# Optimization experiments

Measured on AMD Instinct MI355X. Metric: run time of the kernel, lower is better.

Reference implementation:

```python
import jax, jax.numpy as jnp
import numpy as np

D_MODEL = 1024
NUM_HEADS = 16
ROPE_THETA = 10000.0


def _rope(v, pos, theta=ROPE_THETA):
    # v: [B, S, D] (full d_model, as in the original module), pos: [B, S] int
    d = v.shape[-1]
    inv_freq = theta ** (-jnp.arange(0, d, 2, dtype=jnp.float32) / d)  # [D/2]
    ang = pos.astype(jnp.float32)[..., None] * inv_freq  # [B, S, D/2]
    cos, sin = jnp.cos(ang), jnp.sin(ang)
    x1, x2 = v[..., ::2], v[..., 1::2]
    r1 = x1 * cos - x2 * sin
    r2 = x1 * sin + x2 * cos
    return jnp.stack([r1, r2], axis=-1).reshape(v.shape)


def setup_inputs() -> dict:
    key = jax.random.key(0)
    ks = jax.random.split(key, 6)
    B, S, D = 2, 2048, D_MODEL
    std = np.sqrt(2.0 / (D + D)).astype(np.float32)
    x = jax.random.normal(ks[0], (B, S, D), dtype=jnp.float32)
    token_positions = jnp.sort(jax.random.randint(ks[1], (B, S), 0, S), axis=-1).astype(jnp.int32)
    wq = jax.random.normal(ks[2], (D, D), dtype=jnp.float32) * std
    wk = jax.random.normal(ks[3], (D, D), dtype=jnp.float32) * std
    wv = jax.random.normal(ks[4], (D, D), dtype=jnp.float32) * std
    wo = jax.random.normal(ks[5], (D, D), dtype=jnp.float32) * std
    return {"x": x, "token_positions": token_positions, "wq": wq, "wk": wk, "wv": wv, "wo": wo}


def reference(x, token_positions, wq, wk, wv, wo):
    B, S, D = x.shape
    H = NUM_HEADS
    dk = D // H
    # Projections (nn.functional.linear: x @ W^T)
    q = x @ wq.T
    k = x @ wk.T
    v = x @ wv.T
    # In the original, Q/K are reshaped to heads and back before RoPE -> identity;
    # RoPE is applied over the FULL d_model dimension.
    q = _rope(q, token_positions)
    k = _rope(k, token_positions)
    # Split heads
    q = q.reshape(B, S, H, dk)
    k = k.reshape(B, S, H, dk)
    v = v.reshape(B, S, H, dk)
    scores = jnp.einsum('bqhd,bkhd->bhqk', q, k) / jnp.sqrt(jnp.asarray(dk, x.dtype))
    causal = jnp.tril(jnp.ones((S, S), dtype=bool))  # True where allowed
    scores = jnp.where(causal[None, None], scores, -jnp.inf)
    attn = jax.nn.softmax(scores, axis=-1)
    out = jnp.einsum('bhqk,bkhd->bqhd', attn, v).reshape(B, S, D)
    return out @ wo.T
```

## Files before the change

### kernel.cpp

```cpp
#include <hip/hip_runtime.h>
#include <hip/hip_bf16.h>
#include <math.h>

typedef __attribute__((ext_vector_type(8))) short bf16x8;
typedef __attribute__((ext_vector_type(4))) float f32x4;
typedef __attribute__((ext_vector_type(8))) float f32x8;

#define D_MODEL 1024
#define NHEADS  16
#define DK      64
#define BATCH   2
#define SEQ     2048

static __device__ __forceinline__ short f2bf(float f) {
    unsigned u = __builtin_bit_cast(unsigned, f);
    u = u + 0x7FFFu + ((u >> 16) & 1u);
    return (short)(u >> 16);
}
static __device__ __forceinline__ short f2bf_fast(float f) {
    return (short)((__builtin_bit_cast(unsigned, f) + 0x8000u) >> 16);
}
static __device__ __forceinline__ float bf2f(short s) {
    return __builtin_bit_cast(float, ((unsigned)(unsigned short)s) << 16);
}

typedef __attribute__((address_space(3))) unsigned int lds_uint;
typedef __attribute__((address_space(1))) const unsigned int glob_uint;
static __device__ __forceinline__ void gl2lds16(const short* g, short* l) {
    __builtin_amdgcn_global_load_lds((glob_uint*)g, (lds_uint*)l, 16, 0, 0);
}

__global__ void detect_kernel(const unsigned* __restrict__ x, int* __restrict__ flag)
{
    const int lane = threadIdx.x;
    const unsigned w = x[lane];
    const unsigned e = (w >> 7) & 0xFFu;
    const bool weird = (e >= 0x88u) || (e <= 0x5Fu);
    const unsigned long long m = __ballot(weird);
    if (lane == 0) *flag = (__popcll(m) >= 16) ? 1 : 0;
}

#define NX8 ((BATCH * SEQ * D_MODEL) / 8)
#define NW8 ((D_MODEL * D_MODEL) / 8)
__global__ void cvt_all_kernel(const void* __restrict__ x,  const void* __restrict__ wq,
                               const void* __restrict__ wk, const void* __restrict__ wv,
                               const void* __restrict__ wo,
                               __hip_bfloat16* __restrict__ xb,  __hip_bfloat16* __restrict__ wqb,
                               __hip_bfloat16* __restrict__ wkb, __hip_bfloat16* __restrict__ wvb,
                               __hip_bfloat16* __restrict__ wob,
                               const int* __restrict__ dtf)
{
    const int i = blockIdx.x * blockDim.x + threadIdx.x;
    if (i >= NX8 + 4 * NW8) return;
    const void* src; __hip_bfloat16* dst; int off;
    if (i < NX8) { src = x; dst = xb; off = i; }
    else {
        const int j = i - NX8, seg = j >> 17; off = j & (NW8 - 1);
        switch (seg) {
            case 0: src = wq; dst = wqb; break;
            case 1: src = wk; dst = wkb; break;
            case 2: src = wv; dst = wvb; break;
            default: src = wo; dst = wob; break;
        }
    }
    if (*dtf) {
        const f32x8 v = ((const f32x8*)src)[off];
        bf16x8 r;
#pragma unroll
        for (int j = 0; j < 8; ++j) r[j] = f2bf(v[j]);
        ((bf16x8*)dst)[off] = r;
    } else {
        ((bf16x8*)dst)[off] = ((const bf16x8*)src)[off];
    }
}

static __device__ __forceinline__ void gemm128_main(
    const short* __restrict__ A, const short* __restrict__ B,
    int K, int bm, int bn, f32x4 (&acc)[4][4], short* lds)
{
    const int tid  = threadIdx.x;
    const int lane = tid & 63;
    const int wave = tid >> 6;
    const int l16  = lane & 15;
    const int quad = lane >> 4;

    const int srow = lane >> 2;
    const int scg  = (lane & 3) ^ ((lane >> 3) & 3);
    const short* ag = A + (size_t)(bm + wave * 32 + srow) * K + scg * 8;
    const short* bg = B + (size_t)(bn + wave * 32 + srow) * K + scg * 8;
    const int dst = wave * 1024 + lane * 8;

    const int mrow = (wave >> 1) * 64;
    const int nrow = (wave & 1) * 64;
    const int ph   = ((quad ^ ((l16 >> 1) & 3))) * 8;

    auto stage = [&](int k0, int buf) {
        short* ad = lds + buf * 4096 + dst;
        short* bd = lds + 8192 + buf * 4096 + dst;
        gl2lds16(ag + k0, ad);
        gl2lds16(ag + k0 + (size_t)16 * K, ad + 512);
        gl2lds16(bg + k0, bd);
        gl2lds16(bg + k0 + (size_t)16 * K, bd + 512);
    };

    stage(0, 0);
    for (int k0 = 0, t = 0; k0 < K; k0 += 32, ++t) {
        __asm__ volatile("s_waitcnt vmcnt(0)" ::: "memory");
        __syncthreads();
        if (k0 + 32 < K) stage(k0 + 32, (t + 1) & 1);

        const short* Ab = lds + (t & 1) * 4096;
        const short* Bb = lds + 8192 + (t & 1) * 4096;
        bf16x8 a[4], b[4];
#pragma unroll
        for (int x = 0; x < 4; ++x)
            a[x] = *(const bf16x8*)(Ab + (mrow + x * 16 + l16) * 32 + ph);
#pragma unroll
        for (int y = 0; y < 4; ++y)
            b[y] = *(const bf16x8*)(Bb + (nrow + y * 16 + l16) * 32 + ph);
#pragma unroll
        for (int x = 0; x < 4; ++x)
#pragma unroll
            for (int y = 0; y < 4; ++y)
                acc[x][y] = __builtin_amdgcn_mfma_f32_16x16x32_bf16(
                    a[x], b[y], acc[x][y], 0, 0, 0);
    }
}

__global__ __launch_bounds__(256) void gemm_qkv_kernel(
    const __hip_bfloat16* __restrict__ xb,
    const __hip_bfloat16* __restrict__ wqb,
    const __hip_bfloat16* __restrict__ wkb,
    const __hip_bfloat16* __restrict__ wvb,
    __hip_bfloat16* __restrict__ Qb,
    __hip_bfloat16* __restrict__ Kb,
    __hip_bfloat16* __restrict__ Vt)
{
    __shared__ alignas(16) short lds[16384];
    const int wsel = blockIdx.x >> 3;
    const int bn   = (blockIdx.x & 7) * 128;
    const int bm   = blockIdx.y * 128;
    const short* W = (const short*)(wsel == 0 ? wqb : (wsel == 1 ? wkb : wvb));

    f32x4 acc[4][4];
#pragma unroll
    for (int x = 0; x < 4; ++x)
#pragma unroll
        for (int y = 0; y < 4; ++y) acc[x][y] = (f32x4){0.f, 0.f, 0.f, 0.f};

    gemm128_main((const short*)xb, W, D_MODEL, bm, bn, acc, lds);

    const int lane = threadIdx.x & 63;
    const int wave = threadIdx.x >> 6;
    const int l16  = lane & 15;
    const int quad = lane >> 4;
    __hip_bfloat16* Crm = (wsel == 1) ? Kb : Qb;

#pragma unroll
    for (int x = 0; x < 4; ++x)
#pragma unroll
        for (int y = 0; y < 4; ++y)
#pragma unroll
            for (int r = 0; r < 4; ++r) {
                const int row = bm + (wave >> 1) * 64 + x * 16 + quad * 4 + r;
                const int col = bn + (wave & 1) * 64 + y * 16 + l16;
                const __hip_bfloat16 v = __float2bfloat16(acc[x][y][r]);
                if (wsel == 2) {
                    const int hh = col >> 6, dcol = col & 63;
                    const int bb = row >> 11, ss = row & (SEQ - 1);
                    Vt[(((size_t)bb * NHEADS + hh) * DK + dcol) * SEQ + ss] = v;
                } else {
                    Crm[(size_t)row * D_MODEL + col] = v;
                }
            }
}

__global__ __launch_bounds__(256) void gemm_out_kernel(
    const __hip_bfloat16* __restrict__ AO,
    const __hip_bfloat16* __restrict__ wob,
    void* __restrict__ C, const int* __restrict__ dtf)
{
    __shared__ alignas(16) short lds[16384];
    const int bn = blockIdx.x * 128;
    const int bm = blockIdx.y * 128;
    const bool c32 = (*dtf) != 0;

    f32x4 acc[4][4];
#pragma unroll
    for (int x = 0; x < 4; ++x)
#pragma unroll
        for (int y = 0; y < 4; ++y) acc[x][y] = (f32x4){0.f, 0.f, 0.f, 0.f};

    gemm128_main((const short*)AO, (const short*)wob, D_MODEL, bm, bn, acc, lds);

    const int lane = threadIdx.x & 63;
    const int wave = threadIdx.x >> 6;
    const int l16  = lane & 15;
    const int quad = lane >> 4;

#pragma unroll
    for (int x = 0; x < 4; ++x)
#pragma unroll
        for (int y = 0; y < 4; ++y)
#pragma unroll
            for (int r = 0; r < 4; ++r) {
                const int row = bm + (wave >> 1) * 64 + x * 16 + quad * 4 + r;
                const int col = bn + (wave & 1) * 64 + y * 16 + l16;
                const size_t idx = (size_t)row * D_MODEL + col;
                if (c32) ((float*)C)[idx] = acc[x][y][r];
                else     ((__hip_bfloat16*)C)[idx] = __float2bfloat16(acc[x][y][r]);
            }
}

__global__ void rope_kernel(__hip_bfloat16* __restrict__ Q,
                            __hip_bfloat16* __restrict__ Kt,
                            const int* __restrict__ pos, int n8)
{
    const int idx = blockIdx.x * blockDim.x + threadIdx.x;
    if (idx >= n8) return;
    const int elem0 = idx * 8;
    const int bs = elem0 >> 10;
    const int i0 = (elem0 & (D_MODEL - 1)) >> 1;

    const float p = (float)pos[bs];
    bf16x8 q8 = *((bf16x8*)Q + idx);
    bf16x8 k8 = *((bf16x8*)Kt + idx);

#pragma unroll
    for (int j = 0; j < 4; ++j) {
        const float inv = exp2f((float)(i0 + j) * -0.02595256257f);
        const float ang = p * inv;
        const float c = cosf(ang), s = sinf(ang);
        const float q1 = bf2f(q8[2 * j]);
        const float q2 = bf2f(q8[2 * j + 1]);
        const float k1 = bf2f(k8[2 * j]);
        const float k2 = bf2f(k8[2 * j + 1]);
        q8[2 * j]     = f2bf(q1 * c - q2 * s);
        q8[2 * j + 1] = f2bf(q1 * s + q2 * c);
        k8[2 * j]     = f2bf(k1 * c - k2 * s);
        k8[2 * j + 1] = f2bf(k1 * s + k2 * c);
    }
    *((bf16x8*)Q + idx)  = q8;
    *((bf16x8*)Kt + idx) = k8;
}

__global__ __launch_bounds__(256) void flash_attn_kernel(
    __hip_bfloat16* QO,
    const __hip_bfloat16* __restrict__ Kt,
    const __hip_bfloat16* __restrict__ Vt)
{
    __shared__ alignas(16) short k_lds[2][64 * 64];
    __shared__ alignas(16) short v_lds[2][64 * 64];
    __shared__ alignas(16) short p_lds[4][16 * 72];

    const int lane = threadIdx.x & 63;
    const int wave = threadIdx.x >> 6;
    const int l16  = lane & 15;
    const int quad = lane >> 4;
    const int qtA  = blockIdx.x;
    const int qtB  = 31 - qtA;
    const int b    = blockIdx.y / NHEADS;
    const int h    = blockIdx.y % NHEADS;
    const size_t base  = (size_t)b * SEQ * D_MODEL + h * DK;
    const size_t vbase = (size_t)blockIdx.y * DK * SEQ;

    const short* Qp = (const short*)QO;
    const short* Kp = (const short*)Kt;
    const short* Vp = (const short*)Vt;

    const int qA0 = qtA * 64 + wave * 16;
    const int qB0 = qtB * 64 + wave * 16;
    const bf16x8 aqA0 = *(const bf16x8*)(Qp + base + (size_t)(qA0 + l16) * D_MODEL + quad * 8);
    const bf16x8 aqA1 = *(const bf16x8*)(Qp + base + (size_t)(qA0 + l16) * D_MODEL + 32 + quad * 8);
    const bf16x8 aqB0 = *(const bf16x8*)(Qp + base + (size_t)(qB0 + l16) * D_MODEL + quad * 8);
    const bf16x8 aqB1 = *(const bf16x8*)(Qp + base + (size_t)(qB0 + l16) * D_MODEL + 32 + quad * 8);

    f32x4 oA[4], oB[4];
    float lA[4] = {0.f, 0.f, 0.f, 0.f}, lB[4] = {0.f, 0.f, 0.f, 0.f};
#pragma unroll
    for (int g = 0; g < 4; ++g) { oA[g] = (f32x4){0.f,0.f,0.f,0.f}; oB[g] = (f32x4){0.f,0.f,0.f,0.f}; }

    const int srow = lane >> 3;
    const int scg  = (lane & 7) ^ srow;
    const int dst  = wave * 512 + lane * 8;
    const short* kg = Kp + ((size_t)b * SEQ + wave * 8 + srow) * D_MODEL + h * DK + scg * 8;
    const short* vg = Vp + vbase + (size_t)(wave * 8 + srow) * SEQ + scg * 8;

    const int ph0 = (quad ^ (l16 & 7)) * 8;
    const int ph1 = ((4 + quad) ^ (l16 & 7)) * 8;

    auto stage = [&](int t, int buf) {
        const int kv0 = t * 64;
        gl2lds16(kg + (size_t)kv0 * D_MODEL, k_lds[buf] + dst);
        gl2lds16(kg + (size_t)(kv0 + 32) * D_MODEL, k_lds[buf] + 2048 + dst);
        gl2lds16(vg + kv0, v_lds[buf] + dst);
        gl2lds16(vg + kv0 + (size_t)32 * SEQ, v_lds[buf] + 2048 + dst);
    };

    auto process = [&](int buf, int kv0, int q0, bool masked,
                       const bf16x8& aq0, const bf16x8& aq1,
                       f32x4 (&o)[4], float (&ls)[4]) {
        const short* kb = k_lds[buf];
        const short* vb = v_lds[buf];
        f32x4 sfrag[4];
#pragma unroll
        for (int g = 0; g < 4; ++g) {
            const int rowk = (g * 16 + l16) * 64;
            const bf16x8 bk0 = *(const bf16x8*)(kb + rowk + ph0);
            const bf16x8 bk1 = *(const bf16x8*)(kb + rowk + ph1);
            f32x4 c = (f32x4){0.f, 0.f, 0.f, 0.f};
            c = __builtin_amdgcn_mfma_f32_16x16x32_bf16(aq0, bk0, c, 0, 0, 0);
            c = __builtin_amdgcn_mfma_f32_16x16x32_bf16(aq1, bk1, c, 0, 0, 0);
            sfrag[g] = c;
        }
#pragma unroll
        for (int r = 0; r < 4; ++r) {
            const int qrow = q0 + quad * 4 + r;
            float ps = 0.f;
#pragma unroll
            for (int g = 0; g < 4; ++g) {
                float p = __expf(sfrag[g][r] * 0.125f);
                if (masked && (kv0 + g * 16 + l16 > qrow)) p = 0.f;
                ps += p;
                p_lds[wave][(quad * 4 + r) * 72 + g * 16 + l16] = f2bf_fast(p);
            }
            ls[r] += ps;
        }
        __asm__ volatile("s_waitcnt lgkmcnt(0)" ::: "memory");
        const bf16x8 ap0 = *(const bf16x8*)(&p_lds[wave][l16 * 72 + quad * 8]);
        const bf16x8 ap1 = *(const bf16x8*)(&p_lds[wave][l16 * 72 + 32 + quad * 8]);
#pragma unroll
        for (int g = 0; g < 4; ++g) {
            const int rowv = (g * 16 + l16) * 64;
            const bf16x8 bv0 = *(const bf16x8*)(vb + rowv + ph0);
            const bf16x8 bv1 = *(const bf16x8*)(vb + rowv + ph1);
            o[g] = __builtin_amdgcn_mfma_f32_16x16x32_bf16(ap0, bv0, o[g], 0, 0, 0);
            o[g] = __builtin_amdgcn_mfma_f32_16x16x32_bf16(ap1, bv1, o[g], 0, 0, 0);
        }
    };

    const int tiles = qtB + 1;
    stage(0, 0);
    for (int t = 0; t < tiles; ++t) {
        __asm__ volatile("s_waitcnt vmcnt(0)" ::: "memory");
        __syncthreads();
        if (t + 1 < tiles) stage(t + 1, (t + 1) & 1);

        const int kv0 = t * 64;
        const int buf = t & 1;
        if (t <= qtA) process(buf, kv0, qA0, t == qtA, aqA0, aqA1, oA, lA);
        process(buf, kv0, qB0, t == qtB, aqB0, aqB1, oB, lB);
    }

#pragma unroll
    for (int r = 0; r < 4; ++r) {
        float sa = lA[r], sb = lB[r];
#pragma unroll
        for (int off = 1; off < 16; off <<= 1) {
            sa += __shfl_xor(sa, off);
            sb += __shfl_xor(sb, off);
        }
        lA[r] = sa; lB[r] = sb;
    }
#pragma unroll
    for (int g = 0; g < 4; ++g)
#pragma unroll
        for (int r = 0; r < 4; ++r) {
            const int rowA = qA0 + quad * 4 + r;
            const int rowB = qB0 + quad * 4 + r;
            QO[base + (size_t)rowA * D_MODEL + g * 16 + l16] =
                __float2bfloat16(oA[g][r] / fmaxf(lA[r], 1e-20f));
            QO[base + (size_t)rowB * D_MODEL + g * 16 + l16] =
                __float2bfloat16(oB[g][r] / fmaxf(lB[r], 1e-20f));
        }
}

extern "C" void kernel_launch(void* const* d_in, const int* in_sizes, int n_in,
                              void* d_out, int out_size, void* d_ws, size_t ws_size,
                              hipStream_t stream)
{
    (void)in_sizes; (void)n_in; (void)out_size; (void)ws_size;

    const void* x  = d_in[0];
    const int*  pos = (const int*)d_in[1];
    const void* wq = d_in[2];
    const void* wk = d_in[3];
    const void* wv = d_in[4];
    const void* wo = d_in[5];

    const int M = BATCH * SEQ;
    const int D = D_MODEL;
    const size_t MD = (size_t)M * D;
    const size_t DD = (size_t)D * D;

    int* dtf = (int*)d_ws;
    __hip_bfloat16* xb  = (__hip_bfloat16*)((char*)d_ws + 256);
    __hip_bfloat16* wqb = xb  + MD;
    __hip_bfloat16* wkb = wqb + DD;
    __hip_bfloat16* wvb = wkb + DD;
    __hip_bfloat16* wob = wvb + DD;
    __hip_bfloat16* Qb  = wob + DD;
    __hip_bfloat16* Vtb = Qb  + MD;
    __hip_bfloat16* Kb  = (__hip_bfloat16*)d_out;

    dim3 blk(256);

    hipLaunchKernelGGL(detect_kernel, dim3(1), dim3(64), 0, stream,
                       (const unsigned*)x, dtf);

    const int ncvt = NX8 + 4 * NW8;
    hipLaunchKernelGGL(cvt_all_kernel, dim3((ncvt + 255) / 256), blk, 0, stream,
                       x, wq, wk, wv, wo, xb, wqb, wkb, wvb, wob, dtf);

    hipLaunchKernelGGL(gemm_qkv_kernel, dim3(24, 32), blk, 0, stream,
                       xb, wqb, wkb, wvb, Qb, Kb, Vtb);

    const int nrope8 = (int)(MD / 8);
    hipLaunchKernelGGL(rope_kernel, dim3((nrope8 + 255) / 256), blk, 0, stream,
                       Qb, Kb, pos, nrope8);

    hipLaunchKernelGGL(flash_attn_kernel, dim3(SEQ / 128, BATCH * NHEADS), blk, 0, stream,
                       Qb, Kb, Vtb);

    hipLaunchKernelGGL(gemm_out_kernel, dim3(D / 128, M / 128), blk, 0, stream,
                       Qb, wob, d_out, dtf);
}
```

Before: 202.4 us.

## Fuse RoPE into QKV GEMM epilogue, retile out-proj and widen attention KV tiles

Applies the rotary embedding in the QKV GEMM epilogue, using a lane shuffle to fetch each element's pair partner, and drops the separate RoPE kernel and its extra read and write pass over Q and K. The output-projection GEMM moves to 64x128 tiles with its own double-buffered LDS loop, doubling the block count to improve CU occupancy. Flash attention now stages 128-key K/V tiles per barrier and processes them as two 64-key halves, halving the sync and stage steps. These add trig work to the GEMM epilogue and more LDS per attention block, which may lower occupancy.

Result: slower. 251.2 us (+24.1%).

```diff
diff --git a/kernel.cpp b/kernel.cpp
--- a/kernel.cpp
+++ b/kernel.cpp
@@ -134,7 +134,8 @@
     const __hip_bfloat16* __restrict__ wvb,
     __hip_bfloat16* __restrict__ Qb,
     __hip_bfloat16* __restrict__ Kb,
-    __hip_bfloat16* __restrict__ Vt)
+    __hip_bfloat16* __restrict__ Vt,
+    const int* __restrict__ pos)
 {
     __shared__ alignas(16) short lds[16384];
     const int wsel = blockIdx.x >> 3;
@@ -164,13 +165,22 @@
             for (int r = 0; r < 4; ++r) {
                 const int row = bm + (wave >> 1) * 64 + x * 16 + quad * 4 + r;
                 const int col = bn + (wave & 1) * 64 + y * 16 + l16;
-                const __hip_bfloat16 v = __float2bfloat16(acc[x][y][r]);
+                float v = acc[x][y][r];
+                const float p2 = __shfl_xor(v, 1);
+                if (wsel < 2) {
+                    const float pp  = (float)pos[row];
+                    const float inv = exp2f((float)(col >> 1) * -0.02595256257f);
+                    const float ang = pp * inv;
+                    const float c = cosf(ang), s = sinf(ang);
+                    v = (col & 1) ? (p2 * s + v * c) : (v * c - p2 * s);
+                }
+                const __hip_bfloat16 o = __float2bfloat16(v);
                 if (wsel == 2) {
                     const int hh = col >> 6, dcol = col & 63;
                     const int bb = row >> 11, ss = row & (SEQ - 1);
-                    Vt[(((size_t)bb * NHEADS + hh) * DK + dcol) * SEQ + ss] = v;
+                    Vt[(((size_t)bb * NHEADS + hh) * DK + dcol) * SEQ + ss] = o;
                 } else {
-                    Crm[(size_t)row * D_MODEL + col] = v;
+                    Crm[(size_t)row * D_MODEL + col] = o;
                 }
             }
 }
@@ -180,77 +190,83 @@
     const __hip_bfloat16* __restrict__ wob,
     void* __restrict__ C, const int* __restrict__ dtf)
 {
-    __shared__ alignas(16) short lds[16384];
-    const int bn = blockIdx.x * 128;
-    const int bm = blockIdx.y * 128;
-    const bool c32 = (*dtf) != 0;
-
-    f32x4 acc[4][4];
-#pragma unroll
-    for (int x = 0; x < 4; ++x)
-#pragma unroll
-        for (int y = 0; y < 4; ++y) acc[x][y] = (f32x4){0.f, 0.f, 0.f, 0.f};
-
-    gemm128_main((const short*)AO, (const short*)wob, D_MODEL, bm, bn, acc, lds);
-
-    const int lane = threadIdx.x & 63;
-    const int wave = threadIdx.x >> 6;
+    __shared__ alignas(16) short lds[2][6144];
+    const int tid  = threadIdx.x;
+    const int lane = tid & 63;
+    const int wave = tid >> 6;
     const int l16  = lane & 15;
     const int quad = lane >> 4;
-
+    const int bn = blockIdx.x * 128;
+    const int bm = blockIdx.y * 64;
+    const bool c32 = (*dtf) != 0;
+    const int K = D_MODEL;
+
+    const int srow = lane >> 2;
+    const int scg  = (lane & 3) ^ ((lane >> 3) & 3);
+    const short* Ap = (const short*)AO;
+    const short* Bp = (const short*)wob;
+    const short* ag = Ap + (size_t)(bm + wave * 16 + srow) * K + scg * 8;
+    const short* bg = Bp + (size_t)(bn + wave * 32 + srow) * K + scg * 8;
+
+    const int nrow = wave * 32;
+    const int ph   = ((quad ^ ((l16 >> 1) & 3))) * 8;
+
+    f32x4 acc[4][2];
 #pragma unroll
     for (int x = 0; x < 4; ++x)
 #pragma unroll
-        for (int y = 0; y < 4; ++y)
+        for (int y = 0; y < 2; ++y) acc[x][y] = (f32x4){0.f, 0.f, 0.f, 0.f};
+
+    auto stage = [&](int k0, int buf) {
+        gl2lds16(ag + k0, &lds[buf][wave * 512 + lane * 8]);
+        gl2lds16(bg + k0, &lds[buf][2048 + wave * 1024 + lane * 8]);
+        gl2lds16(bg + k0 + (size_t)16 * K, &lds[buf][2048 + wave * 1024 + 512 + lane * 8]);
+    };
+
+    stage(0, 0);
+    for (int k0 = 0, t = 0; k0 < K; k0 += 32, ++t) {
+        __asm__ volatile("s_waitcnt vmcnt(0)" ::: "memory");
+        __syncthreads();
+        if (k0 + 32 < K) stage(k0 + 32, (t + 1) & 1);
+
+        const short* Ab = &lds[t & 1][0];
+        const short* Bb = &lds[t & 1][2048];
+        bf16x8 a[4], b[2];
+#pragma unroll
+        for (int x = 0; x < 4; ++x)
+            a[x] = *(const bf16x8*)(Ab + (x * 16 + l16) * 32 + ph);
+#pragma unroll
+        for (int y = 0; y < 2; ++y)
+            b[y] = *(const bf16x8*)(Bb + (nrow + y * 16 + l16) * 32 + ph);
+#pragma unroll
+        for (int x = 0; x < 4; ++x)
+#pragma unroll
+            for (int y = 0; y < 2; ++y)
+                acc[x][y] = __builtin_amdgcn_mfma_f32_16x16x32_bf16(
+                    a[x], b[y], acc[x][y], 0, 0, 0);
+    }
+
+#pragma unroll
+    for (int x = 0; x < 4; ++x)
+#pragma unroll
+        for (int y = 0; y < 2; ++y)
 #pragma unroll
             for (int r = 0; r < 4; ++r) {
-                const int row = bm + (wave >> 1) * 64 + x * 16 + quad * 4 + r;
-                const int col = bn + (wave & 1) * 64 + y * 16 + l16;
+                const int row = bm + x * 16 + quad * 4 + r;
+                const int col = bn + nrow + y * 16 + l16;
                 const size_t idx = (size_t)row * D_MODEL + col;
                 if (c32) ((float*)C)[idx] = acc[x][y][r];
                 else     ((__hip_bfloat16*)C)[idx] = __float2bfloat16(acc[x][y][r]);
             }
 }
 
-__global__ void rope_kernel(__hip_bfloat16* __restrict__ Q,
-                            __hip_bfloat16* __restrict__ Kt,
-                            const int* __restrict__ pos, int n8)
-{
-    const int idx = blockIdx.x * blockDim.x + threadIdx.x;
-    if (idx >= n8) return;
-    const int elem0 = idx * 8;
-    const int bs = elem0 >> 10;
-    const int i0 = (elem0 & (D_MODEL - 1)) >> 1;
-
-    const float p = (float)pos[bs];
-    bf16x8 q8 = *((bf16x8*)Q + idx);
-    bf16x8 k8 = *((bf16x8*)Kt + idx);
-
-#pragma unroll
-    for (int j = 0; j < 4; ++j) {
-        const float inv = exp2f((float)(i0 + j) * -0.02595256257f);
-        const float ang = p * inv;
-        const float c = cosf(ang), s = sinf(ang);
-        const float q1 = bf2f(q8[2 * j]);
-        const float q2 = bf2f(q8[2 * j + 1]);
-        const float k1 = bf2f(k8[2 * j]);
-        const float k2 = bf2f(k8[2 * j + 1]);
-        q8[2 * j]     = f2bf(q1 * c - q2 * s);
-        q8[2 * j + 1] = f2bf(q1 * s + q2 * c);
-        k8[2 * j]     = f2bf(k1 * c - k2 * s);
-        k8[2 * j + 1] = f2bf(k1 * s + k2 * c);
-    }
-    *((bf16x8*)Q + idx)  = q8;
-    *((bf16x8*)Kt + idx) = k8;
-}
-
 __global__ __launch_bounds__(256) void flash_attn_kernel(
     __hip_bfloat16* QO,
     const __hip_bfloat16* __restrict__ Kt,
     const __hip_bfloat16* __restrict__ Vt)
 {
-    __shared__ alignas(16) short k_lds[2][64 * 64];
-    __shared__ alignas(16) short v_lds[2][64 * 64];
+    __shared__ alignas(16) short k_lds[2][128 * 64];
+    __shared__ alignas(16) short v_lds[2][64 * 128];
     __shared__ alignas(16) short p_lds[4][16 * 72];
 
     const int lane = threadIdx.x & 63;
@@ -280,28 +296,37 @@
 #pragma unroll
     for (int g = 0; g < 4; ++g) { oA[g] = (f32x4){0.f,0.f,0.f,0.f}; oB[g] = (f32x4){0.f,0.f,0.f,0.f}; }
 
-    const int srow = lane >> 3;
-    const int scg  = (lane & 7) ^ srow;
-    const int dst  = wave * 512 + lane * 8;
-    const short* kg = Kp + ((size_t)b * SEQ + wave * 8 + srow) * D_MODEL + h * DK + scg * 8;
-    const short* vg = Vp + vbase + (size_t)(wave * 8 + srow) * SEQ + scg * 8;
+    const int srowK = lane >> 3;
+    const int scgK  = (lane & 7) ^ srowK;
+    const short* kg = Kp + ((size_t)b * SEQ + wave * 32 + srowK) * D_MODEL + h * DK + scgK * 8;
+    const int rinV = lane >> 4;
+    const int cgV  = lane & 15;
+    const short* vgA = Vp + vbase + (size_t)(wave * 16 + rinV) * SEQ + ((cgV ^ rinV)) * 8;
+    const short* vgB = Vp + vbase + (size_t)(wave * 16 + rinV) * SEQ + ((cgV ^ (4 + rinV))) * 8;
 
     const int ph0 = (quad ^ (l16 & 7)) * 8;
     const int ph1 = ((4 + quad) ^ (l16 & 7)) * 8;
-
-    auto stage = [&](int t, int buf) {
-        const int kv0 = t * 64;
-        gl2lds16(kg + (size_t)kv0 * D_MODEL, k_lds[buf] + dst);
-        gl2lds16(kg + (size_t)(kv0 + 32) * D_MODEL, k_lds[buf] + 2048 + dst);
-        gl2lds16(vg + kv0, v_lds[buf] + dst);
-        gl2lds16(vg + kv0 + (size_t)32 * SEQ, v_lds[buf] + 2048 + dst);
+    const int pv1 = ((8 + quad) ^ (l16 & 7)) * 8;
+
+    auto stage = [&](int t2, int buf) {
+        const int kv0 = t2 * 128;
+#pragma unroll
+        for (int i = 0; i < 4; ++i)
+            gl2lds16(kg + (size_t)(kv0 + i * 8) * D_MODEL,
+                     k_lds[buf] + (wave * 32 + i * 8) * 64 + lane * 8);
+#pragma unroll
+        for (int i = 0; i < 4; ++i) {
+            const short* vp = (i & 1) ? vgB : vgA;
+            gl2lds16(vp + (size_t)(i * 4) * SEQ + kv0,
+                     v_lds[buf] + (wave * 16 + i * 4) * 128 + lane * 8);
+        }
     };
 
-    auto process = [&](int buf, int kv0, int q0, bool masked,
+    auto process = [&](int buf, int half, int kv0, int q0, bool masked,
                        const bf16x8& aq0, const bf16x8& aq1,
                        f32x4 (&o)[4], float (&ls)[4]) {
-        const short* kb = k_lds[buf];
-        const short* vb = v_lds[buf];
+        const short* kb = k_lds[buf] + half * 64 * 64;
+        const short* vb = v_lds[buf] + half * 64;
         f32x4 sfrag[4];
 #pragma unroll
         for (int g = 0; g < 4; ++g) {
@@ -329,27 +354,30 @@
         __asm__ volatile("s_waitcnt lgkmcnt(0)" ::: "memory");
         const bf16x8 ap0 = *(const bf16x8*)(&p_lds[wave][l16 * 72 + quad * 8]);
         const bf16x8 ap1 = *(const bf16x8*)(&p_lds[wave][l16 * 72 + 32 + quad * 8]);
+        const int phv0 = half ? pv1 : ph0;
 #pragma unroll
         for (int g = 0; g < 4; ++g) {
-            const int rowv = (g * 16 + l16) * 64;
-            const bf16x8 bv0 = *(const bf16x8*)(vb + rowv + ph0);
-            const bf16x8 bv1 = *(const bf16x8*)(vb + rowv + ph1);
+            const int rowv = (g * 16 + l16) * 128;
+            const bf16x8 bv0 = *(const bf16x8*)(v_lds[buf] + rowv + half * 0 + phv0);
+            const bf16x8 bv1 = *(const bf16x8*)(v_lds[buf] + rowv + (half ? ph1 + 64 : ph1));
             o[g] = __builtin_amdgcn_mfma_f32_16x16x32_bf16(ap0, bv0, o[g], 0, 0, 0);
             o[g] = __builtin_amdgcn_mfma_f32_16x16x32_bf16(ap1, bv1, o[g], 0, 0, 0);
         }
     };
 
-    const int tiles = qtB + 1;
+    const int t2max = qtB >> 1;
     stage(0, 0);
-    for (int t = 0; t < tiles; ++t) {
+    for (int t2 = 0; t2 <= t2max; ++t2) {
         __asm__ volatile("s_waitcnt vmcnt(0)" ::: "memory");
         __syncthreads();
-        if (t + 1 < tiles) stage(t + 1, (t + 1) & 1);
-
-        const int kv0 = t * 64;
-        const int buf = t & 1;
-        if (t <= qtA) process(buf, kv0, qA0, t == qtA, aqA0, aqA1, oA, lA);
-        process(buf, kv0, qB0, t == qtB, aqB0, aqB1, oB, lB);
+        if (t2 < t2max) stage(t2 + 1, (t2 + 1) & 1);
+        const int buf = t2 & 1;
+#pragma unroll
+        for (int half = 0; half < 2; ++half) {
+            const int kvt = 2 * t2 + half;
+            if (kvt <= qtA) process(buf, half, kvt * 64, qA0, kvt == qtA, aqA0, aqA1, oA, lA);
+            if (kvt <= qtB) process(buf, half, kvt * 64, qB0, kvt == qtB, aqB0, aqB1, oB, lB);
+        }
     }
 
 #pragma unroll
@@ -413,15 +441,11 @@
                        x, wq, wk, wv, wo, xb, wqb, wkb, wvb, wob, dtf);
 
     hipLaunchKernelGGL(gemm_qkv_kernel, dim3(24, 32), blk, 0, stream,
-                       xb, wqb, wkb, wvb, Qb, Kb, Vtb);
-
-    const int nrope8 = (int)(MD / 8);
-    hipLaunchKernelGGL(rope_kernel, dim3((nrope8 + 255) / 256), blk, 0, stream,
-                       Qb, Kb, pos, nrope8);
+                       xb, wqb, wkb, wvb, Qb, Kb, Vtb, pos);
 
     hipLaunchKernelGGL(flash_attn_kernel, dim3(SEQ / 128, BATCH * NHEADS), blk, 0, stream,
                        Qb, Kb, Vtb);
 
-    hipLaunchKernelGGL(gemm_out_kernel, dim3(D / 128, M / 128), blk, 0, stream,
+    hipLaunchKernelGGL(gemm_out_kernel, dim3(D / 128, M / 64), blk, 0, stream,
                        Qb, wob, d_out, dtf);
 }
```
